# Kernel tuning notes

Hardware: AMD Instinct MI355X
Metric: run time of the kernel (lower is better)

## Reference

```python
import jax, jax.numpy as jnp
import numpy as np

U = 100000   # num_users
I = 50000    # num_items
N = U + I    # total nodes
D = 64       # embed_size
L = 3        # n_layers
E = 2000000  # num edges
EPS = 1e-12  # F.normalize default eps


def setup_inputs() -> dict:
    key = jax.random.key(0)
    k1, k2, k3, k4 = jax.random.split(key, 4)
    user_emb = jax.random.normal(k1, (U, D), dtype=jnp.float32) * 0.1
    item_emb = jax.random.normal(k2, (I, D), dtype=jnp.float32) * 0.1
    rows = jax.random.randint(k3, (E,), 0, N, dtype=jnp.int32)
    cols = jax.random.randint(k4, (E,), 0, N, dtype=jnp.int32)
    return {"user_emb": user_emb, "item_emb": item_emb, "rows": rows, "cols": cols}


def _spmm(vals, rows, cols, x):
    # sparse [N,N] @ dense [N,D] via gather + segment reduce
    return jax.ops.segment_sum(vals[:, None] * x[cols], rows, num_segments=N)


def _l2norm(x):
    return x / jnp.maximum(jnp.linalg.norm(x, axis=1, keepdims=True), EPS)


def reference(user_emb, item_emb, rows, cols):
    emb0 = jnp.concatenate([user_emb, item_emb], axis=0)  # [N, D]

    # laplacian_adj: G = D^-1/2 A D^-1/2 on the same edge set
    deg = jax.ops.segment_sum(jnp.ones((E,), emb0.dtype), rows, num_segments=N)
    d_is = jnp.where(deg > 0, deg ** -0.5, 0.0)
    g_vals = d_is[rows] * d_is[cols]  # [E]

    cur = emb0
    acc = emb0
    user_fine, item_fine = [], []
    for _ in range(L):
        gnn = _spmm(g_vals, rows, cols, cur)  # [N, D]
        # fine_laplacian_adj: cosine-sim edge scores, row-normalized
        gr = _l2norm(gnn[rows])
        gc = _l2norm(gnn[cols])
        scores = (jnp.sum(gr * gc, axis=1) + 1.0) * 0.5  # [E] in [0,1]
        rowsum = jax.ops.segment_sum(scores, rows, num_segments=N)
        d_inv = jnp.where(rowsum > 0, 1.0 / rowsum, 0.0)
        fine = _spmm(d_inv[rows] * scores, rows, cols, cur)  # [N, D]
        cur = gnn + fine
        acc = acc + cur
        user_fine.append(fine[:U])
        item_fine.append(fine[U:])

    u_embs = acc[:U]
    i_embs = acc[U:]
    return (u_embs, i_embs, jnp.stack(user_fine, 0), jnp.stack(item_fine, 0))
```

## Files before the change

kernel.cpp:

```cpp
#include <hip/hip_runtime.h>

namespace {

typedef unsigned short u16;

constexpr int Un = 100000;
constexpr int In = 50000;
constexpr int Nn = 150000;
constexpr int D  = 64;
constexpr int Ln = 3;
constexpr int En = 2000000;
constexpr int CHUNK = 1024;
constexpr int NB = (Nn + CHUNK - 1) / CHUNK;

__device__ __forceinline__ float bf2f(u16 u) {
    return __uint_as_float(((unsigned)u) << 16);
}
__device__ __forceinline__ u16 f2bf(float f) {
    unsigned u = __float_as_uint(f);
    unsigned r = (u + 0x7FFFu + ((u >> 16) & 1u)) >> 16;
    return (u16)r;
}
__device__ __forceinline__ float bflo(unsigned u) {
    return __uint_as_float(u << 16);
}
__device__ __forceinline__ float bfhi(unsigned u) {
    return __uint_as_float(u & 0xFFFF0000u);
}
__device__ __forceinline__ void bf8(const uint4 q, float* o) {
    o[0] = bflo(q.x); o[1] = bfhi(q.x);
    o[2] = bflo(q.y); o[3] = bfhi(q.y);
    o[4] = bflo(q.z); o[5] = bfhi(q.z);
    o[6] = bflo(q.w); o[7] = bfhi(q.w);
}
__device__ __forceinline__ unsigned pack2(float lo, float hi) {
    return (unsigned)f2bf(lo) | ((unsigned)f2bf(hi) << 16);
}

__global__ void count_kernel(const int* __restrict__ rows, int* __restrict__ deg,
                             int* __restrict__ eoff) {
    int e = blockIdx.x * blockDim.x + threadIdx.x;
    if (e < En) eoff[e] = atomicAdd(&deg[rows[e]], 1);
}

__global__ void scan_partial(const int* __restrict__ deg, float* __restrict__ d_is,
                             int* __restrict__ bsum) {
    int tid = threadIdx.x;
    int base = blockIdx.x * CHUNK + tid * 4;
    int s = 0;
#pragma unroll
    for (int i = 0; i < 4; ++i) {
        int idx = base + i;
        if (idx < Nn) {
            int d = deg[idx];
            s += d;
            d_is[idx] = d > 0 ? rsqrtf((float)d) : 0.f;
        }
    }
    __shared__ int sh[256];
    sh[tid] = s;
    __syncthreads();
    for (int o = 128; o > 0; o >>= 1) {
        if (tid < o) sh[tid] += sh[tid + o];
        __syncthreads();
    }
    if (tid == 0) bsum[blockIdx.x] = sh[0];
}

__global__ void scan_top(int* __restrict__ bsum, int* __restrict__ row_ptr) {
    __shared__ int sh[256];
    int tid = threadIdx.x;
    int v = (tid < NB) ? bsum[tid] : 0;
    sh[tid] = v;
    __syncthreads();
    for (int o = 1; o < 256; o <<= 1) {
        int t = (tid >= o) ? sh[tid - o] : 0;
        __syncthreads();
        sh[tid] += t;
        __syncthreads();
    }
    if (tid < NB) bsum[tid] = sh[tid] - v;
    if (tid == 255) row_ptr[Nn] = sh[255];
}

__global__ void scan_final(const int* __restrict__ deg, const int* __restrict__ bsum,
                           int* __restrict__ row_ptr) {
    int tid = threadIdx.x;
    int base = blockIdx.x * CHUNK + tid * 4;
    int v[4];
    int ts = 0;
#pragma unroll
    for (int i = 0; i < 4; ++i) {
        int idx = base + i;
        v[i] = (idx < Nn) ? deg[idx] : 0;
        ts += v[i];
    }
    __shared__ int sh[256];
    sh[tid] = ts;
    __syncthreads();
    for (int o = 1; o < 256; o <<= 1) {
        int t = (tid >= o) ? sh[tid - o] : 0;
        __syncthreads();
        sh[tid] += t;
        __syncthreads();
    }
    int excl = bsum[blockIdx.x] + sh[tid] - ts;
#pragma unroll
    for (int i = 0; i < 4; ++i) {
        int idx = base + i;
        if (idx < Nn) row_ptr[idx] = excl;
        excl += v[i];
    }
}

__global__ void fill_kernel(const int* __restrict__ rows, const int* __restrict__ cols,
                            const int* __restrict__ row_ptr, const int* __restrict__ eoff,
                            int* __restrict__ col_s) {
    int e = blockIdx.x * blockDim.x + threadIdx.x;
    if (e >= En) return;
    col_s[row_ptr[rows[e]] + eoff[e]] = cols[e];
}

__global__ void init_kernel(const float* __restrict__ ue, const float* __restrict__ ie,
                            float* __restrict__ out, u16* __restrict__ cur) {
    int i = (blockIdx.x * 256 + threadIdx.x) * 4;
    if (i >= Nn * D) return;
    const float* src = (i < Un * D) ? (ue + i) : (ie + (i - Un * D));
    float4 v = *(const float4*)src;
    *(float4*)(out + i) = v;
    ushort4 q;
    q.x = f2bf(v.x); q.y = f2bf(v.y); q.z = f2bf(v.z); q.w = f2bf(v.w);
    *(ushort4*)(cur + i) = q;
}

__global__ __launch_bounds__(256) void spmm_gnn(const u16* __restrict__ A, u16* __restrict__ B,
                                                const int* __restrict__ row_ptr,
                                                const int* __restrict__ col_s,
                                                const float* __restrict__ d_is,
                                                float* __restrict__ inv_norm) {
    int r = (blockIdx.x * 256 + threadIdx.x) >> 6;
    if (r >= Nn) return;
    int lane = threadIdx.x & 63;
    int g = lane >> 3, l = lane & 7;
    int s = row_ptr[r], t = row_ptr[r + 1];
    float dr = d_is[r];
    float a[8] = {0.f, 0.f, 0.f, 0.f, 0.f, 0.f, 0.f, 0.f};
    int nit = (t - s + 7) >> 3;
#pragma unroll 2
    for (int i = 0; i < nit; ++i) {
        int j = s + i * 8 + g;
        bool valid = j < t;
        int jc = valid ? j : (t - 1);
        int c = col_s[jc];
        float v = valid ? dr * d_is[c] : 0.f;
        uint4 q = *(const uint4*)(A + (size_t)c * D + l * 8);
        float x[8];
        bf8(q, x);
#pragma unroll
        for (int k = 0; k < 8; ++k) a[k] += v * x[k];
    }
#pragma unroll
    for (int k = 0; k < 8; ++k) {
        a[k] += __shfl_xor(a[k], 8);
        a[k] += __shfl_xor(a[k], 16);
        a[k] += __shfl_xor(a[k], 32);
    }
    float sq = 0.f;
#pragma unroll
    for (int k = 0; k < 8; ++k) sq += a[k] * a[k];
    sq += __shfl_xor(sq, 1); sq += __shfl_xor(sq, 2); sq += __shfl_xor(sq, 4);
    if (g == 0) {
        uint4 o;
        o.x = pack2(a[0], a[1]); o.y = pack2(a[2], a[3]);
        o.z = pack2(a[4], a[5]); o.w = pack2(a[6], a[7]);
        *(uint4*)(B + (size_t)r * D + l * 8) = o;
        if (l == 0) inv_norm[r] = 1.f / fmaxf(sqrtf(sq), 1e-12f);
    }
}

__global__ __launch_bounds__(256) void score_fine_kernel(const u16* __restrict__ A,
                                                         const u16* __restrict__ B,
                                                         u16* __restrict__ C,
                                                         const float* __restrict__ inv_norm,
                                                         const int* __restrict__ row_ptr,
                                                         const int* __restrict__ col_s,
                                                         float* __restrict__ out, int layer) {
    int r = (blockIdx.x * 256 + threadIdx.x) >> 6;
    if (r >= Nn) return;
    int lane = threadIdx.x & 63;
    int g = lane >> 3, l = lane & 7;
    int s = row_ptr[r], t = row_ptr[r + 1];
    uint4 qb = *(const uint4*)(B + (size_t)r * D + l * 8);
    float b[8];
    bf8(qb, b);
    float ir = inv_norm[r];
    float rowsum = 0.f;
    float f[8] = {0.f, 0.f, 0.f, 0.f, 0.f, 0.f, 0.f, 0.f};
    int nit = (t - s + 7) >> 3;
#pragma unroll 2
    for (int i = 0; i < nit; ++i) {
        int j = s + i * 8 + g;
        bool valid = j < t;
        int jc = valid ? j : (t - 1);
        int c = col_s[jc];
        uint4 qc = *(const uint4*)(B + (size_t)c * D + l * 8);
        uint4 qa = *(const uint4*)(A + (size_t)c * D + l * 8);
        float inc = inv_norm[c];
        float x[8];
        bf8(qc, x);
        float d = b[0] * x[0] + b[1] * x[1] + b[2] * x[2] + b[3] * x[3]
                + b[4] * x[4] + b[5] * x[5] + b[6] * x[6] + b[7] * x[7];
        d += __shfl_xor(d, 1); d += __shfl_xor(d, 2); d += __shfl_xor(d, 4);
        float sc = (d * ir * inc + 1.f) * 0.5f;
        if (!valid) sc = 0.f;
        rowsum += sc;
        float y[8];
        bf8(qa, y);
#pragma unroll
        for (int k = 0; k < 8; ++k) f[k] += sc * y[k];
    }
    rowsum += __shfl_xor(rowsum, 8);
    rowsum += __shfl_xor(rowsum, 16);
    rowsum += __shfl_xor(rowsum, 32);
#pragma unroll
    for (int k = 0; k < 8; ++k) {
        f[k] += __shfl_xor(f[k], 8);
        f[k] += __shfl_xor(f[k], 16);
        f[k] += __shfl_xor(f[k], 32);
    }
    float di = rowsum > 0.f ? 1.f / rowsum : 0.f;
#pragma unroll
    for (int k = 0; k < 8; ++k) f[k] *= di;
    if (g == 0) {
        size_t ro = (size_t)r * D + l * 8;
        float cn[8];
#pragma unroll
        for (int k = 0; k < 8; ++k) cn[k] = b[k] + f[k];
        uint4 qn;
        qn.x = pack2(cn[0], cn[1]); qn.y = pack2(cn[2], cn[3]);
        qn.z = pack2(cn[4], cn[5]); qn.w = pack2(cn[6], cn[7]);
        *(uint4*)(C + ro) = qn;
        float4* av = (float4*)(out + ro);
        float4 a0 = av[0], a1 = av[1];
        a0.x += cn[0]; a0.y += cn[1]; a0.z += cn[2]; a0.w += cn[3];
        a1.x += cn[4]; a1.y += cn[5]; a1.z += cn[6]; a1.w += cn[7];
        av[0] = a0; av[1] = a1;
        size_t fo;
        if (r < Un)
            fo = (size_t)Nn * D + (size_t)layer * Un * D + (size_t)r * D + l * 8;
        else
            fo = (size_t)Nn * D + (size_t)Ln * Un * D + (size_t)layer * In * D
                 + (size_t)(r - Un) * D + l * 8;
        float4 f0, f1;
        f0.x = f[0]; f0.y = f[1]; f0.z = f[2]; f0.w = f[3];
        f1.x = f[4]; f1.y = f[5]; f1.z = f[6]; f1.w = f[7];
        ((float4*)(out + fo))[0] = f0;
        ((float4*)(out + fo))[1] = f1;
    }
}

}

extern "C" void kernel_launch(void* const* d_in, const int* in_sizes, int n_in,
                              void* d_out, int out_size, void* d_ws, size_t ws_size,
                              hipStream_t stream) {
    const float* user_emb = (const float*)d_in[0];
    const float* item_emb = (const float*)d_in[1];
    const int* rows = (const int*)d_in[2];
    const int* cols = (const int*)d_in[3];
    float* out = (float*)d_out;

    char* ws = (char*)d_ws;
    size_t off = 0;
    auto alloc = [&](size_t bytes) -> void* {
        void* p = ws + off;
        off += (bytes + 255) & ~size_t(255);
        return p;
    };
    u16*   buf0    = (u16*)  alloc((size_t)Nn * D * 2);
    u16*   buf1    = (u16*)  alloc((size_t)Nn * D * 2);
    u16*   buf2    = (u16*)  alloc((size_t)Nn * D * 2);
    int*   col_s   = (int*)  alloc((size_t)En * 4);
    int*   deg     = (int*)  alloc((size_t)Nn * 4);
    int*   row_ptr = (int*)  alloc((size_t)(Nn + 1) * 4);
    float* d_is    = (float*)alloc((size_t)Nn * 4);
    float* inv_norm= (float*)alloc((size_t)Nn * 4);
    int*   bsum    = (int*)  alloc(4096);
    int*   eoff    = (int*)buf1;
    (void)ws_size; (void)in_sizes; (void)n_in; (void)out_size;

    hipMemsetAsync(deg, 0, (size_t)Nn * 4, stream);

    init_kernel<<<(Nn * D / 4 + 255) / 256, 256, 0, stream>>>(user_emb, item_emb, out, buf0);

    const int EB = (En + 255) / 256;
    count_kernel<<<EB, 256, 0, stream>>>(rows, deg, eoff);
    scan_partial<<<NB, 256, 0, stream>>>(deg, d_is, bsum);
    scan_top<<<1, 256, 0, stream>>>(bsum, row_ptr);
    scan_final<<<NB, 256, 0, stream>>>(deg, bsum, row_ptr);
    fill_kernel<<<EB, 256, 0, stream>>>(rows, cols, row_ptr, eoff, col_s);

    const int RB = Nn / 4;
    u16* P = buf0;
    u16* Q = buf1;
    u16* R = buf2;
    for (int l = 0; l < Ln; ++l) {
        spmm_gnn<<<RB, 256, 0, stream>>>(P, Q, row_ptr, col_s, d_is, inv_norm);
        score_fine_kernel<<<RB, 256, 0, stream>>>(P, Q, R, inv_norm, row_ptr, col_s, out, l);
        u16* t0 = P, *t1 = Q, *t2 = R;
        P = t2; Q = t0; R = t1;
    }
}
```

Baseline: 814.2 us.

## Store pre-normalized gnn rows and byte-offset column indices; use packed FMA and DPP

spmm_gnn now writes a second bf16 copy of each gnn row already scaled by its inverse L2 norm. The score kernel then reads the normalized neighbor rows directly and drops the per-edge inv_norm gather and multiplies. Column indices are stored pre-shifted as byte offsets, so the d_is and row addresses come from one value. The inner loops are split into full groups of eight plus a masked remainder, and use v_pk_fma_f32 and DPP row reductions instead of scalar FMAs and shuffles. This costs an extra bf16 buffer, changes rounding because normalization happens before bf16 quantization, and the byte offsets rely on 32-bit arithmetic staying in range.

```diff
diff --git a/kernel.cpp b/kernel.cpp
--- a/kernel.cpp
+++ b/kernel.cpp
@@ -3,6 +3,7 @@
 namespace {
 
 typedef unsigned short u16;
+typedef __attribute__((__ext_vector_type__(2))) float f32x2;
 
 constexpr int Un = 100000;
 constexpr int In = 50000;
@@ -13,9 +14,6 @@
 constexpr int CHUNK = 1024;
 constexpr int NB = (Nn + CHUNK - 1) / CHUNK;
 
-__device__ __forceinline__ float bf2f(u16 u) {
-    return __uint_as_float(((unsigned)u) << 16);
-}
 __device__ __forceinline__ u16 f2bf(float f) {
     unsigned u = __float_as_uint(f);
     unsigned r = (u + 0x7FFFu + ((u >> 16) & 1u)) >> 16;
@@ -27,14 +25,31 @@
 __device__ __forceinline__ float bfhi(unsigned u) {
     return __uint_as_float(u & 0xFFFF0000u);
 }
-__device__ __forceinline__ void bf8(const uint4 q, float* o) {
-    o[0] = bflo(q.x); o[1] = bfhi(q.x);
-    o[2] = bflo(q.y); o[3] = bfhi(q.y);
-    o[4] = bflo(q.z); o[5] = bfhi(q.z);
-    o[6] = bflo(q.w); o[7] = bfhi(q.w);
-}
 __device__ __forceinline__ unsigned pack2(float lo, float hi) {
     return (unsigned)f2bf(lo) | ((unsigned)f2bf(hi) << 16);
+}
+
+__device__ __forceinline__ f32x2 pkfma(f32x2 a, f32x2 b, f32x2 c) {
+    f32x2 d;
+    asm("v_pk_fma_f32 %0, %1, %2, %3" : "=v"(d) : "v"(a), "v"(b), "v"(c));
+    return d;
+}
+
+__device__ __forceinline__ float dpp_add8(float x) {
+    x += __uint_as_float((unsigned)__builtin_amdgcn_update_dpp(
+        0, (int)__float_as_uint(x), 0xB1, 0xF, 0xF, true));
+    x += __uint_as_float((unsigned)__builtin_amdgcn_update_dpp(
+        0, (int)__float_as_uint(x), 0x4E, 0xF, 0xF, true));
+    x += __uint_as_float((unsigned)__builtin_amdgcn_update_dpp(
+        0, (int)__float_as_uint(x), 0x141, 0xF, 0xF, true));
+    return x;
+}
+
+__device__ __forceinline__ void unp8(uint4 q, f32x2* o) {
+    o[0].x = bflo(q.x); o[0].y = bfhi(q.x);
+    o[1].x = bflo(q.y); o[1].y = bfhi(q.y);
+    o[2].x = bflo(q.z); o[2].y = bfhi(q.z);
+    o[3].x = bflo(q.w); o[3].y = bfhi(q.w);
 }
 
 __global__ void count_kernel(const int* __restrict__ rows, int* __restrict__ deg,
@@ -115,10 +130,10 @@
 
 __global__ void fill_kernel(const int* __restrict__ rows, const int* __restrict__ cols,
                             const int* __restrict__ row_ptr, const int* __restrict__ eoff,
-                            int* __restrict__ col_s) {
+                            int* __restrict__ col_off) {
     int e = blockIdx.x * blockDim.x + threadIdx.x;
     if (e >= En) return;
-    col_s[row_ptr[rows[e]] + eoff[e]] = cols[e];
+    col_off[row_ptr[rows[e]] + eoff[e]] = cols[e] << 7;
 }
 
 __global__ void init_kernel(const float* __restrict__ ue, const float* __restrict__ ie,
@@ -133,32 +148,54 @@
     *(ushort4*)(cur + i) = q;
 }
 
-__global__ __launch_bounds__(256) void spmm_gnn(const u16* __restrict__ A, u16* __restrict__ B,
+__global__ __launch_bounds__(256) void spmm_gnn(const u16* __restrict__ A_,
+                                                u16* __restrict__ Q_,
+                                                u16* __restrict__ Qn_,
                                                 const int* __restrict__ row_ptr,
-                                                const int* __restrict__ col_s,
-                                                const float* __restrict__ d_is,
-                                                float* __restrict__ inv_norm) {
+                                                const int* __restrict__ col_off,
+                                                const float* __restrict__ d_is) {
     int r = (blockIdx.x * 256 + threadIdx.x) >> 6;
     if (r >= Nn) return;
     int lane = threadIdx.x & 63;
     int g = lane >> 3, l = lane & 7;
+    unsigned l16 = (unsigned)l * 16u;
+    const char* pA = (const char*)A_;
+    const char* pd = (const char*)d_is;
     int s = row_ptr[r], t = row_ptr[r + 1];
     float dr = d_is[r];
-    float a[8] = {0.f, 0.f, 0.f, 0.f, 0.f, 0.f, 0.f, 0.f};
-    int nit = (t - s + 7) >> 3;
+    f32x2 z; z.x = 0.f; z.y = 0.f;
+    f32x2 a2[4] = {z, z, z, z};
+    int deg = t - s;
+    int nfull = deg >> 3;
+    int rem = deg & 7;
+    int jb = s + g;
 #pragma unroll 2
-    for (int i = 0; i < nit; ++i) {
-        int j = s + i * 8 + g;
-        bool valid = j < t;
-        int jc = valid ? j : (t - 1);
-        int c = col_s[jc];
-        float v = valid ? dr * d_is[c] : 0.f;
-        uint4 q = *(const uint4*)(A + (size_t)c * D + l * 8);
-        float x[8];
-        bf8(q, x);
-#pragma unroll
-        for (int k = 0; k < 8; ++k) a[k] += v * x[k];
-    }
+    for (int i = 0; i < nfull; ++i) {
+        unsigned off = (unsigned)col_off[jb + i * 8];
+        float dv = *(const float*)(pd + (off >> 5));
+        float v = dr * dv;
+        uint4 q = *(const uint4*)(pA + (off + l16));
+        f32x2 x2[4];
+        unp8(q, x2);
+        f32x2 v2; v2.x = v; v2.y = v;
+#pragma unroll
+        for (int p = 0; p < 4; ++p) a2[p] = pkfma(v2, x2[p], a2[p]);
+    }
+    if (rem) {
+        bool valid = g < rem;
+        int jc = valid ? (jb + nfull * 8) : s;
+        unsigned off = (unsigned)col_off[jc];
+        float dv = *(const float*)(pd + (off >> 5));
+        float v = valid ? dr * dv : 0.f;
+        uint4 q = *(const uint4*)(pA + (off + l16));
+        f32x2 x2[4];
+        unp8(q, x2);
+        f32x2 v2; v2.x = v; v2.y = v;
+#pragma unroll
+        for (int p = 0; p < 4; ++p) a2[p] = pkfma(v2, x2[p], a2[p]);
+    }
+    float a[8] = {a2[0].x, a2[0].y, a2[1].x, a2[1].y,
+                  a2[2].x, a2[2].y, a2[3].x, a2[3].y};
 #pragma unroll
     for (int k = 0; k < 8; ++k) {
         a[k] += __shfl_xor(a[k], 8);
@@ -167,58 +204,94 @@
     }
     float sq = 0.f;
 #pragma unroll
-    for (int k = 0; k < 8; ++k) sq += a[k] * a[k];
-    sq += __shfl_xor(sq, 1); sq += __shfl_xor(sq, 2); sq += __shfl_xor(sq, 4);
+    for (int k = 0; k < 8; ++k) sq = fmaf(a[k], a[k], sq);
+    sq = dpp_add8(sq);
     if (g == 0) {
+        float ir = 1.f / fmaxf(sqrtf(sq), 1e-12f);
+        unsigned ro = ((unsigned)r << 7) + l16;
         uint4 o;
         o.x = pack2(a[0], a[1]); o.y = pack2(a[2], a[3]);
         o.z = pack2(a[4], a[5]); o.w = pack2(a[6], a[7]);
-        *(uint4*)(B + (size_t)r * D + l * 8) = o;
-        if (l == 0) inv_norm[r] = 1.f / fmaxf(sqrtf(sq), 1e-12f);
-    }
-}
-
-__global__ __launch_bounds__(256) void score_fine_kernel(const u16* __restrict__ A,
-                                                         const u16* __restrict__ B,
-                                                         u16* __restrict__ C,
-                                                         const float* __restrict__ inv_norm,
+        *(uint4*)((char*)Q_ + ro) = o;
+        uint4 on;
+        on.x = pack2(a[0] * ir, a[1] * ir); on.y = pack2(a[2] * ir, a[3] * ir);
+        on.z = pack2(a[4] * ir, a[5] * ir); on.w = pack2(a[6] * ir, a[7] * ir);
+        *(uint4*)((char*)Qn_ + ro) = on;
+    }
+}
+
+__global__ __launch_bounds__(256) void score_fine_kernel(const u16* __restrict__ A_,
+                                                         const u16* __restrict__ Q_,
+                                                         const u16* __restrict__ Qn_,
+                                                         u16* __restrict__ C_,
                                                          const int* __restrict__ row_ptr,
-                                                         const int* __restrict__ col_s,
+                                                         const int* __restrict__ col_off,
                                                          float* __restrict__ out, int layer) {
     int r = (blockIdx.x * 256 + threadIdx.x) >> 6;
     if (r >= Nn) return;
     int lane = threadIdx.x & 63;
     int g = lane >> 3, l = lane & 7;
+    unsigned l16 = (unsigned)l * 16u;
+    const char* pQn = (const char*)Qn_;
+    const char* pA  = (const char*)A_;
     int s = row_ptr[r], t = row_ptr[r + 1];
-    uint4 qb = *(const uint4*)(B + (size_t)r * D + l * 8);
-    float b[8];
-    bf8(qb, b);
-    float ir = inv_norm[r];
+    unsigned ro = ((unsigned)r << 7) + l16;
+    uint4 qbn = *(const uint4*)(pQn + ro);
+    f32x2 b2[4];
+    unp8(qbn, b2);
+    f32x2 z; z.x = 0.f; z.y = 0.f;
+    f32x2 facc[4] = {z, z, z, z};
     float rowsum = 0.f;
-    float f[8] = {0.f, 0.f, 0.f, 0.f, 0.f, 0.f, 0.f, 0.f};
-    int nit = (t - s + 7) >> 3;
+    int deg = t - s;
+    int nfull = deg >> 3;
+    int rem = deg & 7;
+    int jb = s + g;
 #pragma unroll 2
-    for (int i = 0; i < nit; ++i) {
-        int j = s + i * 8 + g;
-        bool valid = j < t;
-        int jc = valid ? j : (t - 1);
-        int c = col_s[jc];
-        uint4 qc = *(const uint4*)(B + (size_t)c * D + l * 8);
-        uint4 qa = *(const uint4*)(A + (size_t)c * D + l * 8);
-        float inc = inv_norm[c];
-        float x[8];
-        bf8(qc, x);
-        float d = b[0] * x[0] + b[1] * x[1] + b[2] * x[2] + b[3] * x[3]
-                + b[4] * x[4] + b[5] * x[5] + b[6] * x[6] + b[7] * x[7];
-        d += __shfl_xor(d, 1); d += __shfl_xor(d, 2); d += __shfl_xor(d, 4);
-        float sc = (d * ir * inc + 1.f) * 0.5f;
+    for (int i = 0; i < nfull; ++i) {
+        unsigned off = (unsigned)col_off[jb + i * 8];
+        unsigned vo = off + l16;
+        uint4 qx = *(const uint4*)(pQn + vo);
+        uint4 qy = *(const uint4*)(pA + vo);
+        f32x2 x2[4];
+        unp8(qx, x2);
+        f32x2 d2 = pkfma(b2[0], x2[0], z);
+        d2 = pkfma(b2[1], x2[1], d2);
+        d2 = pkfma(b2[2], x2[2], d2);
+        d2 = pkfma(b2[3], x2[3], d2);
+        float d = dpp_add8(d2.x + d2.y);
+        float sc = fmaf(d, 0.5f, 0.5f);
+        rowsum += sc;
+        f32x2 y2[4];
+        unp8(qy, y2);
+        f32x2 sc2; sc2.x = sc; sc2.y = sc;
+#pragma unroll
+        for (int p = 0; p < 4; ++p) facc[p] = pkfma(sc2, y2[p], facc[p]);
+    }
+    if (rem) {
+        bool valid = g < rem;
+        int jc = valid ? (jb + nfull * 8) : s;
+        unsigned off = (unsigned)col_off[jc];
+        unsigned vo = off + l16;
+        uint4 qx = *(const uint4*)(pQn + vo);
+        uint4 qy = *(const uint4*)(pA + vo);
+        f32x2 x2[4];
+        unp8(qx, x2);
+        f32x2 d2 = pkfma(b2[0], x2[0], z);
+        d2 = pkfma(b2[1], x2[1], d2);
+        d2 = pkfma(b2[2], x2[2], d2);
+        d2 = pkfma(b2[3], x2[3], d2);
+        float d = dpp_add8(d2.x + d2.y);
+        float sc = fmaf(d, 0.5f, 0.5f);
         if (!valid) sc = 0.f;
         rowsum += sc;
-        float y[8];
-        bf8(qa, y);
-#pragma unroll
-        for (int k = 0; k < 8; ++k) f[k] += sc * y[k];
-    }
+        f32x2 y2[4];
+        unp8(qy, y2);
+        f32x2 sc2; sc2.x = sc; sc2.y = sc;
+#pragma unroll
+        for (int p = 0; p < 4; ++p) facc[p] = pkfma(sc2, y2[p], facc[p]);
+    }
+    float f[8] = {facc[0].x, facc[0].y, facc[1].x, facc[1].y,
+                  facc[2].x, facc[2].y, facc[3].x, facc[3].y};
     rowsum += __shfl_xor(rowsum, 8);
     rowsum += __shfl_xor(rowsum, 16);
     rowsum += __shfl_xor(rowsum, 32);
@@ -232,19 +305,22 @@
 #pragma unroll
     for (int k = 0; k < 8; ++k) f[k] *= di;
     if (g == 0) {
-        size_t ro = (size_t)r * D + l * 8;
+        uint4 qb = *(const uint4*)((const char*)Q_ + ro);
+        float b[8] = {bflo(qb.x), bfhi(qb.x), bflo(qb.y), bfhi(qb.y),
+                      bflo(qb.z), bfhi(qb.z), bflo(qb.w), bfhi(qb.w)};
         float cn[8];
 #pragma unroll
         for (int k = 0; k < 8; ++k) cn[k] = b[k] + f[k];
         uint4 qn;
         qn.x = pack2(cn[0], cn[1]); qn.y = pack2(cn[2], cn[3]);
         qn.z = pack2(cn[4], cn[5]); qn.w = pack2(cn[6], cn[7]);
-        *(uint4*)(C + ro) = qn;
-        float4* av = (float4*)(out + ro);
-        float4 a0 = av[0], a1 = av[1];
+        *(uint4*)((char*)C_ + ro) = qn;
+        float* op = out + (size_t)r * D + l * 8;
+        float4 a0 = ((float4*)op)[0], a1 = ((float4*)op)[1];
         a0.x += cn[0]; a0.y += cn[1]; a0.z += cn[2]; a0.w += cn[3];
         a1.x += cn[4]; a1.y += cn[5]; a1.z += cn[6]; a1.w += cn[7];
-        av[0] = a0; av[1] = a1;
+        ((float4*)op)[0] = a0;
+        ((float4*)op)[1] = a1;
         size_t fo;
         if (r < Un)
             fo = (size_t)Nn * D + (size_t)layer * Un * D + (size_t)r * D + l * 8;
@@ -280,13 +356,13 @@
     u16*   buf0    = (u16*)  alloc((size_t)Nn * D * 2);
     u16*   buf1    = (u16*)  alloc((size_t)Nn * D * 2);
     u16*   buf2    = (u16*)  alloc((size_t)Nn * D * 2);
-    int*   col_s   = (int*)  alloc((size_t)En * 4);
+    u16*   buf3    = (u16*)  alloc((size_t)Nn * D * 2);
+    int*   col_off = (int*)  alloc((size_t)(En + 8) * 4);
     int*   deg     = (int*)  alloc((size_t)Nn * 4);
     int*   row_ptr = (int*)  alloc((size_t)(Nn + 1) * 4);
     float* d_is    = (float*)alloc((size_t)Nn * 4);
-    float* inv_norm= (float*)alloc((size_t)Nn * 4);
     int*   bsum    = (int*)  alloc(4096);
-    int*   eoff    = (int*)buf1;
+    int*   eoff    = (int*)buf2;
     (void)ws_size; (void)in_sizes; (void)n_in; (void)out_size;
 
     hipMemsetAsync(deg, 0, (size_t)Nn * 4, stream);
@@ -298,16 +374,14 @@
     scan_partial<<<NB, 256, 0, stream>>>(deg, d_is, bsum);
     scan_top<<<1, 256, 0, stream>>>(bsum, row_ptr);
     scan_final<<<NB, 256, 0, stream>>>(deg, bsum, row_ptr);
-    fill_kernel<<<EB, 256, 0, stream>>>(rows, cols, row_ptr, eoff, col_s);
+    fill_kernel<<<EB, 256, 0, stream>>>(rows, cols, row_ptr, eoff, col_off);
 
     const int RB = Nn / 4;
     u16* P = buf0;
-    u16* Q = buf1;
-    u16* R = buf2;
+    u16* R = buf3;
     for (int l = 0; l < Ln; ++l) {
-        spmm_gnn<<<RB, 256, 0, stream>>>(P, Q, row_ptr, col_s, d_is, inv_norm);
-        score_fine_kernel<<<RB, 256, 0, stream>>>(P, Q, R, inv_norm, row_ptr, col_s, out, l);
-        u16* t0 = P, *t1 = Q, *t2 = R;
-        P = t2; Q = t0; R = t1;
-    }
-}
+        spmm_gnn<<<RB, 256, 0, stream>>>(P, buf1, buf2, row_ptr, col_off, d_is);
+        score_fine_kernel<<<RB, 256, 0, stream>>>(P, buf1, buf2, R, row_ptr, col_off, out, l);
+        u16* tmp = P; P = R; R = tmp;
+    }
+}
```

New measurement: 792.9 us. 1.03x faster.
